# Optimization experiments

Measured on AMD Instinct MI355X. Metric: run time of the kernel, lower is better.

## Reference

```python
import jax, jax.numpy as jnp
from jax import lax
import numpy as np

TEMP = 0.9
TOP_P = 0.95
TOP_K = 50
THRESHOLD = 0.9
MASK_ID = 50256
BLOCK = 128
VOCAB = 50257
GEN = 1024
PROMPT = 512


def setup_inputs() -> dict:
    key = jax.random.key(0)
    k1, k2 = jax.random.split(key)
    logits = jax.random.normal(k1, (1, GEN, VOCAB), dtype=jnp.float32)
    x = jax.random.randint(k2, (1, PROMPT + GEN), 0, VOCAB, dtype=jnp.int32)
    # current block is fully masked -> current_transfer_tokens == BLOCK (static)
    x = x.at[:, PROMPT:PROMPT + BLOCK].set(MASK_ID)
    mask_index = jnp.zeros((1, GEN), dtype=bool).at[:, :BLOCK].set(True)
    return {"i": 0, "x": x, "logits": logits, "mask_index": mask_index,
            "current_block_start": PROMPT, "num_transfer": BLOCK}


def _filter_logits(logits):
    """temperature + top-p + top-k filtering, faithful to torch Sampler."""
    l = logits / TEMP
    neg = jnp.finfo(l.dtype).min
    # top-p: sort descending, cumulative softmax, shifted removal mask, unsort
    sort_idx = jnp.argsort(-l, axis=-1)                       # [1,L,V]
    sorted_l = jnp.take_along_axis(l, sort_idx, axis=-1)
    cum = jnp.cumsum(jax.nn.softmax(sorted_l, axis=-1), axis=-1)
    remove = cum > TOP_P
    remove = jnp.concatenate([jnp.zeros_like(remove[..., :1]), remove[..., :-1]], axis=-1)
    inv = jnp.argsort(sort_idx, axis=-1)                      # inverse permutation
    rm_mask = jnp.take_along_axis(remove, inv, axis=-1)
    l = jnp.where(rm_mask, neg, l)
    # top-k: keep values >= k-th largest
    kth = lax.top_k(l, TOP_K)[0][..., -1:]
    l = jnp.where(l < kth, neg, l)
    return l


def reference(i, x, logits, mask_index, current_block_start, num_transfer):
    l = _filter_logits(logits)                                # [1,GEN,V]
    probs = jax.nn.softmax(l, axis=-1)
    # temperature > 0 -> categorical sample, confidence = prob of sampled token
    x0 = jax.random.categorical(jax.random.key(42), l, axis=-1)          # [1,GEN]
    confidence = jnp.take_along_axis(probs, x0[..., None], axis=-1)[..., 0]
    # scatter into full region: x_[mask]=x0, full_confidence[mask]=conf else -inf
    x_ = jnp.where(mask_index, x0.astype(x.dtype), jnp.asarray(MASK_ID, x.dtype))
    full_conf = jnp.where(mask_index, confidence, -jnp.inf)
    full_conf = full_conf.at[:, BLOCK:].set(-jnp.inf)
    # top-k over positions; index 0 always transferred, rest only if >= threshold
    sel_conf, sel_idx = lax.top_k(full_conf, num_transfer)    # [1,k]
    keep = (sel_conf >= THRESHOLD).at[:, 0].set(True)
    transfer = jnp.zeros(x_.shape, dtype=bool).at[0, sel_idx[0]].set(keep[0])
    region = x[:, current_block_start:]
    new_region = jnp.where(transfer, x_, region)
    x_new = x.at[:, current_block_start:].set(new_region)
    return x_new, full_conf
```

## Files before the change

### kernel.cpp

```cpp
#include <hip/hip_runtime.h>
#include <stdint.h>
#include <math.h>

#define VOCAB 50257
#define GEN 1024
#define PROMPT 512
#define XTOT (PROMPT + GEN)
#define BLOCKQ 128
#define TOPK 50
#define TEMP 0.9f
#define TOPP 0.95f
#define THRESH 0.9f
#define MASK_ID 50256
#define CAND_T 3.0f
#define NEG_SENTINEL (-3.0e38f)

#define NSPLIT 16
#define CHUNK 3144
#define KPT 13
#define MAXCC 48

#define WS_CONF   0
#define WS_X0     512
#define WS_PMAX   1024
#define WS_PSUM   9216
#define WS_CCNT   17408
#define WS_CVAL   25600
#define WS_CIDX   418816
#define WS_NEEDED 812032

__device__ __forceinline__ uint32_t rotl32(uint32_t x, uint32_t d){ return (x<<d)|(x>>(32u-d)); }

__device__ __forceinline__ bool read_mask(const void* m, int r){
  const uint8_t* b = (const uint8_t*)m;
  bool i32mode = ((b[1] | b[2] | b[3]) == 0);
  return i32mode ? (((const int*)m)[r] != 0) : (b[r] != 0);
}

__device__ void threefry2x32_20(uint32_t k0, uint32_t k1, uint32_t& x0, uint32_t& x1){
  uint32_t ks2 = k0 ^ k1 ^ 0x1BD11BDAu;
  x0 += k0; x1 += k1;
#define RND(r) { x0 += x1; x1 = rotl32(x1, r); x1 ^= x0; }
  RND(13) RND(15) RND(26) RND(6)
  x0 += k1; x1 += ks2 + 1u;
  RND(17) RND(29) RND(16) RND(24)
  x0 += ks2; x1 += k0 + 2u;
  RND(13) RND(15) RND(26) RND(6)
  x0 += k0; x1 += k1 + 3u;
  RND(17) RND(29) RND(16) RND(24)
  x0 += k1; x1 += ks2 + 4u;
  RND(13) RND(15) RND(26) RND(6)
  x0 += ks2; x1 += k0 + 5u;
#undef RND
}

__device__ float gumbel_at(int64_t flat){
  const int64_t N = (int64_t)GEN * VOCAB;
  const int64_t half = N / 2;
  uint32_t a, b; int use_first;
  if (flat < half){ a = (uint32_t)flat; b = (uint32_t)(flat + half); use_first = 1; }
  else            { a = (uint32_t)(flat - half); b = (uint32_t)flat;  use_first = 0; }
  threefry2x32_20(0u, 42u, a, b);
  uint32_t bits = use_first ? a : b;
  uint32_t fb = (bits >> 9) | 0x3F800000u;
  float f = __uint_as_float(fb) - 1.0f;
  float u = (f > 0.0f) ? f : 1.17549435e-38f;
  double t = -log((double)u);
  return (float)(-log(t));
}

__global__ __launch_bounds__(256) void stage1_kernel(
    const float* __restrict__ logits,
    const void* __restrict__ mask,
    float* __restrict__ pmax, float* __restrict__ psum,
    int* __restrict__ ccnt, float* __restrict__ cval, int* __restrict__ cidx)
{
  const int r = blockIdx.x >> 4;
  const int c = blockIdx.x & (NSPLIT - 1);
  const int tid = threadIdx.x;
  const int slot = r * NSPLIT + c;

  if (!read_mask(mask, r)){
    if (tid == 0) ccnt[slot] = 0;
    return;
  }
  const float* row = logits + (size_t)r * VOCAB;
  const int i0 = c * CHUNK;
  const int i1 = min(i0 + CHUNK, VOCAB);

  __shared__ int s_cnt;
  __shared__ float red[256];
  if (tid == 0) s_cnt = 0;
  __syncthreads();

  float v[KPT];
  float m = -INFINITY;
#pragma unroll
  for (int k = 0; k < KPT; k++){
    int i = i0 + tid + k * 256;
    float l = -INFINITY;
    if (i < i1){
      l = row[i] / TEMP;
      if (l >= CAND_T){
        int p = atomicAdd(&s_cnt, 1);
        if (p < MAXCC){
          cval[(size_t)slot * MAXCC + p] = l;
          cidx[(size_t)slot * MAXCC + p] = i;
        }
      }
    }
    v[k] = l;
    m = fmaxf(m, l);
  }

  red[tid] = m;
  __syncthreads();
  for (int s = 128; s > 0; s >>= 1){
    if (tid < s) red[tid] = fmaxf(red[tid], red[tid + s]);
    __syncthreads();
  }
  const float mc = red[0];
  __syncthreads();

  float z = 0.f;
#pragma unroll
  for (int k = 0; k < KPT; k++) z += expf(v[k] - mc);
  red[tid] = z;
  __syncthreads();
  for (int s = 128; s > 0; s >>= 1){
    if (tid < s) red[tid] += red[tid + s];
    __syncthreads();
  }
  if (tid == 0){
    pmax[slot] = mc;
    psum[slot] = red[0];
    ccnt[slot] = min(s_cnt, MAXCC);
  }
}

__global__ __launch_bounds__(256) void stage2_kernel(
    const void* __restrict__ mask,
    const float* __restrict__ pmax, const float* __restrict__ psum,
    const int* __restrict__ ccnt, const float* __restrict__ cval, const int* __restrict__ cidx,
    float* __restrict__ conf_out, int* __restrict__ x0_out)
{
  const int r = blockIdx.x;
  const int tid = threadIdx.x;

  if (!read_mask(mask, r)){
    if (tid == 0){ conf_out[r] = -INFINITY; x0_out[r] = 0; }
    return;
  }

  __shared__ float cv[NSPLIT * MAXCC];
  __shared__ int   cx[NSPLIT * MAXCC];
  __shared__ int   s_off[NSPLIT + 1];
  __shared__ float topv[TOPK];
  __shared__ int   topi[TOPK];
  __shared__ float s_m, s_Z, s_Zf;
  __shared__ int   s_keptN;
  __shared__ float sv[64];
  __shared__ int   si[64];

  if (tid == 0){
    float m = -INFINITY;
    for (int c = 0; c < NSPLIT; c++) m = fmaxf(m, pmax[r * NSPLIT + c]);
    float Z = 0.f;
    for (int c = 0; c < NSPLIT; c++) Z += psum[r * NSPLIT + c] * expf(pmax[r * NSPLIT + c] - m);
    s_m = m; s_Z = Z;
    int off = 0;
    for (int c = 0; c < NSPLIT; c++){ s_off[c] = off; off += min(ccnt[r * NSPLIT + c], MAXCC); }
    s_off[NSPLIT] = off;
  }
  __syncthreads();
  const float mm = s_m;
  const int cnt = s_off[NSPLIT];

  for (int c = 0; c < NSPLIT; c++){
    int base = s_off[c], n = s_off[c + 1] - base;
    for (int j = tid; j < n; j += 256){
      cv[base + j] = cval[(size_t)(r * NSPLIT + c) * MAXCC + j];
      cx[base + j] = cidx[(size_t)(r * NSPLIT + c) * MAXCC + j];
    }
  }
  __syncthreads();

  for (int i = tid; i < cnt; i += 256){
    float v = cv[i]; int ix = cx[i];
    int rank = 0;
    for (int j = 0; j < cnt; j++){
      float vj = cv[j];
      rank += (vj > v) || (vj == v && cx[j] < ix);
    }
    if (rank < TOPK){ topv[rank] = v; topi[rank] = ix; }
  }
  __syncthreads();

  if (tid == 0){
    int kn = min(cnt, TOPK);
    float cum = 0.f;
    int c = kn;
    for (int j = 1; j < kn; j++){
      cum += expf(topv[j - 1] - mm) / s_Z;
      if (cum > TOPP){ c = j; break; }
    }
    int keptN = (c < kn) ? c : kn;
    float Zf = 0.f;
    for (int j = 0; j < keptN; j++) Zf += expf(topv[j] - mm);
    s_keptN = keptN; s_Zf = Zf;
  }
  __syncthreads();

  const int keptN = s_keptN;
  if (tid < 64){ sv[tid] = -INFINITY; si[tid] = 0x7FFFFFFF; }
  __syncthreads();
  if (tid < keptN){
    int64_t flat = (int64_t)r * VOCAB + topi[tid];
    float g = gumbel_at(flat);
    sv[tid] = topv[tid] + g;
    si[tid] = topi[tid];
  }
  __syncthreads();

  if (tid == 0){
    float best = -INFINITY; int bi = 0x7FFFFFFF; float wl = 0.f;
    for (int j = 0; j < keptN; j++){
      float s = sv[j]; int ix = si[j];
      if (s > best || (s == best && ix < bi)){ best = s; bi = ix; wl = topv[j]; }
    }
    if (keptN <= 0){ conf_out[r] = 0.f; x0_out[r] = 0; }
    else {
      conf_out[r] = expf(wl - mm) / s_Zf;
      x0_out[r] = bi;
    }
  }
}

__global__ __launch_bounds__(256) void row_kernel(
    const float* __restrict__ logits,
    const void* __restrict__ mask,
    float* __restrict__ conf_out, int* __restrict__ x0_out)
{
  const int r = blockIdx.x;
  const int tid = threadIdx.x;

  __shared__ float cval[768];
  __shared__ int   cidx[768];
  __shared__ int   ccount;
  __shared__ float red[256];
  __shared__ float topv[TOPK];
  __shared__ int   topi[TOPK];
  __shared__ float s_m, s_Z, s_Zf;
  __shared__ int   s_keptN;
  __shared__ float sv[64];
  __shared__ int   si[64];

  if (!read_mask(mask, r)){
    if (tid == 0){ conf_out[r] = -INFINITY; x0_out[r] = 0; }
    return;
  }
  const float* row = logits + (size_t)r * VOCAB;
  if (tid == 0) ccount = 0;
  __syncthreads();

  float m = -INFINITY;
  for (int i = tid; i < VOCAB; i += 256){
    float l = row[i] / TEMP;
    m = fmaxf(m, l);
    if (l >= CAND_T){
      int pos = atomicAdd(&ccount, 1);
      if (pos < 768){ cval[pos] = l; cidx[pos] = i; }
    }
  }
  red[tid] = m;
  __syncthreads();
  for (int s = 128; s > 0; s >>= 1){
    if (tid < s) red[tid] = fmaxf(red[tid], red[tid + s]);
    __syncthreads();
  }
  if (tid == 0) s_m = red[0];
  __syncthreads();
  const float mm = s_m;

  float z = 0.f;
  for (int i = tid; i < VOCAB; i += 256){
    float l = row[i] / TEMP;
    z += expf(l - mm);
  }
  red[tid] = z;
  __syncthreads();
  for (int s = 128; s > 0; s >>= 1){
    if (tid < s) red[tid] += red[tid + s];
    __syncthreads();
  }
  if (tid == 0) s_Z = red[0];
  __syncthreads();

  const int cnt = min(ccount, 768);
  for (int i = tid; i < cnt; i += 256){
    float v = cval[i]; int ix = cidx[i];
    int rank = 0;
    for (int j = 0; j < cnt; j++){
      float vj = cval[j];
      rank += (vj > v) || (vj == v && cidx[j] < ix);
    }
    if (rank < TOPK){ topv[rank] = v; topi[rank] = ix; }
  }
  __syncthreads();

  if (tid == 0){
    int kn = min(cnt, TOPK);
    float cum = 0.f;
    int c = kn;
    for (int j = 1; j < kn; j++){
      cum += expf(topv[j - 1] - mm) / s_Z;
      if (cum > TOPP){ c = j; break; }
    }
    int keptN = (c < kn) ? c : kn;
    float Zf = 0.f;
    for (int j = 0; j < keptN; j++) Zf += expf(topv[j] - mm);
    s_keptN = keptN; s_Zf = Zf;
  }
  __syncthreads();

  const int keptN = s_keptN;
  if (tid < 64){ sv[tid] = -INFINITY; si[tid] = 0x7FFFFFFF; }
  __syncthreads();
  if (tid < keptN){
    int64_t flat = (int64_t)r * VOCAB + topi[tid];
    float g = gumbel_at(flat);
    sv[tid] = topv[tid] + g;
    si[tid] = topi[tid];
  }
  __syncthreads();

  if (tid == 0){
    float best = -INFINITY; int bi = 0x7FFFFFFF; float wl = 0.f;
    for (int j = 0; j < keptN; j++){
      float s = sv[j]; int ix = si[j];
      if (s > best || (s == best && ix < bi)){ best = s; bi = ix; wl = topv[j]; }
    }
    if (keptN <= 0){ conf_out[r] = 0.f; x0_out[r] = 0; }
    else {
      conf_out[r] = expf(wl - mm) / s_Zf;
      x0_out[r] = bi;
    }
  }
}

__global__ __launch_bounds__(256) void finalize_kernel(
    const int* __restrict__ x,
    const void* __restrict__ mask,
    const int* __restrict__ cbs_p, const int* __restrict__ nt_p,
    const float* __restrict__ conf, const int* __restrict__ x0,
    float* __restrict__ out)
{
  __shared__ float fc[BLOCKQ];
  __shared__ uint8_t tr[BLOCKQ];
  const int tid = threadIdx.x;

  if (tid < BLOCKQ) fc[tid] = conf[tid];
  __syncthreads();

  for (int p = tid; p < GEN; p += 256){
    float v = (p < BLOCKQ) ? fc[p] : -INFINITY;
    out[XTOT + p] = isinf(v) ? NEG_SENTINEL : v;
  }

  const int nt  = *nt_p;
  const int cbs = *cbs_p;

  if (tid < BLOCKQ){
    float v = fc[tid];
    int rank = 0;
    for (int q = 0; q < BLOCKQ; q++){
      float w = fc[q];
      rank += (w > v) || (w == v && q < tid);
    }
    bool sel = rank < nt;
    tr[tid] = (uint8_t)(sel && (v >= THRESH || rank == 0));
  }
  __syncthreads();

  for (int k = tid; k < XTOT; k += 256){
    int val = x[k];
    int p = k - cbs;
    if (p >= 0 && p < BLOCKQ && tr[p]){
      val = read_mask(mask, p) ? x0[p] : MASK_ID;
    }
    out[k] = (float)val;
  }
}

extern "C" void kernel_launch(void* const* d_in, const int* in_sizes, int n_in,
                              void* d_out, int out_size, void* d_ws, size_t ws_size,
                              hipStream_t stream)
{
  const int*   x      = (const int*)d_in[1];
  const float* logits = (const float*)d_in[2];
  const void*  mask   = d_in[3];
  const int*   cbs    = (const int*)d_in[4];
  const int*   nt     = (const int*)d_in[5];
  float* out  = (float*)d_out;

  char*  ws   = (char*)d_ws;
  float* conf = (float*)(ws + WS_CONF);
  int*   x0   = (int*)(ws + WS_X0);

  if (ws_size >= WS_NEEDED){
    float* pmax = (float*)(ws + WS_PMAX);
    float* psum = (float*)(ws + WS_PSUM);
    int*   ccnt = (int*)(ws + WS_CCNT);
    float* cval = (float*)(ws + WS_CVAL);
    int*   cidx = (int*)(ws + WS_CIDX);
    hipLaunchKernelGGL(stage1_kernel, dim3(BLOCKQ * NSPLIT), dim3(256), 0, stream,
                       logits, mask, pmax, psum, ccnt, cval, cidx);
    hipLaunchKernelGGL(stage2_kernel, dim3(BLOCKQ), dim3(256), 0, stream,
                       mask, pmax, psum, ccnt, cval, cidx, conf, x0);
  } else {
    hipLaunchKernelGGL(row_kernel, dim3(BLOCKQ), dim3(256), 0, stream,
                       logits, mask, conf, x0);
  }
  hipLaunchKernelGGL(finalize_kernel, dim3(1), dim3(256), 0, stream,
                     x, mask, cbs, nt, conf, x0, out);
}
```

Measured before the change: 60.65 us.

## Fuse split-row stages and finalize into one kernel via last-block atomic counters

Merges the per-chunk partial reduction, the per-row candidate merge and sampling, and the final top-k/transfer step into a single kernel. Each row's last finishing chunk block, found with an atomic counter, does the row merge, and the globally last row does the finalize. A small kernel zeroes the counters first, and the shared-memory tree reductions become wavefront shuffle reductions. This removes inter-kernel launch gaps at the cost of serialised tail work in the last blocks and added fences and atomics.

```diff
diff --git a/kernel.cpp b/kernel.cpp
--- a/kernel.cpp
+++ b/kernel.cpp
@@ -22,12 +22,14 @@
 
 #define WS_CONF   0
 #define WS_X0     512
-#define WS_PMAX   1024
-#define WS_PSUM   9216
-#define WS_CCNT   17408
-#define WS_CVAL   25600
-#define WS_CIDX   418816
-#define WS_NEEDED 812032
+#define WS_ROWCNT 1024
+#define WS_DONE   1536
+#define WS_PMAX   2048
+#define WS_PSUM   10240
+#define WS_CCNT   18432
+#define WS_CVAL   26624
+#define WS_CIDX   419840
+#define WS_NEEDED 813056
 
 __device__ __forceinline__ uint32_t rotl32(uint32_t x, uint32_t d){ return (x<<d)|(x>>(32u-d)); }
 
@@ -69,89 +71,26 @@
   return (float)(-log(t));
 }
 
-__global__ __launch_bounds__(256) void stage1_kernel(
-    const float* __restrict__ logits,
-    const void* __restrict__ mask,
-    float* __restrict__ pmax, float* __restrict__ psum,
-    int* __restrict__ ccnt, float* __restrict__ cval, int* __restrict__ cidx)
+__global__ __launch_bounds__(256) void zero_kernel(int* __restrict__ p){
+  if (threadIdx.x < BLOCKQ + 1) p[threadIdx.x] = 0;
+}
+
+__global__ __launch_bounds__(256) void fused_kernel(
+    const float* __restrict__ logits, const void* __restrict__ mask,
+    const int* __restrict__ x, const int* __restrict__ cbs_p, const int* __restrict__ nt_p,
+    float* __restrict__ out,
+    float* conf, int* x0, int* rowcnt, int* done,
+    float* pmax, float* psum, int* ccnt, float* cval, int* cidx)
 {
-  const int r = blockIdx.x >> 4;
-  const int c = blockIdx.x & (NSPLIT - 1);
+  const int bid = blockIdx.x;
+  const int r = bid >> 4;
+  const int c = bid & (NSPLIT - 1);
   const int tid = threadIdx.x;
-  const int slot = r * NSPLIT + c;
-
-  if (!read_mask(mask, r)){
-    if (tid == 0) ccnt[slot] = 0;
-    return;
-  }
-  const float* row = logits + (size_t)r * VOCAB;
-  const int i0 = c * CHUNK;
-  const int i1 = min(i0 + CHUNK, VOCAB);
-
-  __shared__ int s_cnt;
-  __shared__ float red[256];
-  if (tid == 0) s_cnt = 0;
-  __syncthreads();
-
-  float v[KPT];
-  float m = -INFINITY;
-#pragma unroll
-  for (int k = 0; k < KPT; k++){
-    int i = i0 + tid + k * 256;
-    float l = -INFINITY;
-    if (i < i1){
-      l = row[i] / TEMP;
-      if (l >= CAND_T){
-        int p = atomicAdd(&s_cnt, 1);
-        if (p < MAXCC){
-          cval[(size_t)slot * MAXCC + p] = l;
-          cidx[(size_t)slot * MAXCC + p] = i;
-        }
-      }
-    }
-    v[k] = l;
-    m = fmaxf(m, l);
-  }
-
-  red[tid] = m;
-  __syncthreads();
-  for (int s = 128; s > 0; s >>= 1){
-    if (tid < s) red[tid] = fmaxf(red[tid], red[tid + s]);
-    __syncthreads();
-  }
-  const float mc = red[0];
-  __syncthreads();
-
-  float z = 0.f;
-#pragma unroll
-  for (int k = 0; k < KPT; k++) z += expf(v[k] - mc);
-  red[tid] = z;
-  __syncthreads();
-  for (int s = 128; s > 0; s >>= 1){
-    if (tid < s) red[tid] += red[tid + s];
-    __syncthreads();
-  }
-  if (tid == 0){
-    pmax[slot] = mc;
-    psum[slot] = red[0];
-    ccnt[slot] = min(s_cnt, MAXCC);
-  }
-}
-
-__global__ __launch_bounds__(256) void stage2_kernel(
-    const void* __restrict__ mask,
-    const float* __restrict__ pmax, const float* __restrict__ psum,
-    const int* __restrict__ ccnt, const float* __restrict__ cval, const int* __restrict__ cidx,
-    float* __restrict__ conf_out, int* __restrict__ x0_out)
-{
-  const int r = blockIdx.x;
-  const int tid = threadIdx.x;
-
-  if (!read_mask(mask, r)){
-    if (tid == 0){ conf_out[r] = -INFINITY; x0_out[r] = 0; }
-    return;
-  }
-
+  const int lane = tid & 63;
+  const int wid = tid >> 6;
+
+  __shared__ float lred[4];
+  __shared__ int s_cnt, s_last, s_fin;
   __shared__ float cv[NSPLIT * MAXCC];
   __shared__ int   cx[NSPLIT * MAXCC];
   __shared__ int   s_off[NSPLIT + 1];
@@ -161,89 +100,184 @@
   __shared__ int   s_keptN;
   __shared__ float sv[64];
   __shared__ int   si[64];
-
-  if (tid == 0){
+  __shared__ float fc[BLOCKQ];
+  __shared__ uint8_t tr[BLOCKQ];
+
+  const bool rmask = read_mask(mask, r);
+
+  if (rmask){
+    const float* row = logits + (size_t)r * VOCAB;
+    const int i0 = c * CHUNK;
+    const int i1 = min(i0 + CHUNK, VOCAB);
+    if (tid == 0) s_cnt = 0;
+    __syncthreads();
+
+    float v[KPT];
     float m = -INFINITY;
-    for (int c = 0; c < NSPLIT; c++) m = fmaxf(m, pmax[r * NSPLIT + c]);
-    float Z = 0.f;
-    for (int c = 0; c < NSPLIT; c++) Z += psum[r * NSPLIT + c] * expf(pmax[r * NSPLIT + c] - m);
-    s_m = m; s_Z = Z;
-    int off = 0;
-    for (int c = 0; c < NSPLIT; c++){ s_off[c] = off; off += min(ccnt[r * NSPLIT + c], MAXCC); }
-    s_off[NSPLIT] = off;
-  }
-  __syncthreads();
-  const float mm = s_m;
-  const int cnt = s_off[NSPLIT];
-
-  for (int c = 0; c < NSPLIT; c++){
-    int base = s_off[c], n = s_off[c + 1] - base;
-    for (int j = tid; j < n; j += 256){
-      cv[base + j] = cval[(size_t)(r * NSPLIT + c) * MAXCC + j];
-      cx[base + j] = cidx[(size_t)(r * NSPLIT + c) * MAXCC + j];
-    }
-  }
-  __syncthreads();
-
-  for (int i = tid; i < cnt; i += 256){
-    float v = cv[i]; int ix = cx[i];
+#pragma unroll
+    for (int k = 0; k < KPT; k++){
+      int i = i0 + tid + k * 256;
+      float l = -INFINITY;
+      if (i < i1){
+        l = row[i] / TEMP;
+        if (l >= CAND_T){
+          int p = atomicAdd(&s_cnt, 1);
+          if (p < MAXCC){
+            cval[(size_t)bid * MAXCC + p] = l;
+            cidx[(size_t)bid * MAXCC + p] = i;
+          }
+        }
+      }
+      v[k] = l;
+      m = fmaxf(m, l);
+    }
+#pragma unroll
+    for (int off = 32; off; off >>= 1) m = fmaxf(m, __shfl_xor(m, off));
+    if (lane == 0) lred[wid] = m;
+    __syncthreads();
+    const float mc = fmaxf(fmaxf(lred[0], lred[1]), fmaxf(lred[2], lred[3]));
+    float z = 0.f;
+#pragma unroll
+    for (int k = 0; k < KPT; k++) z += expf(v[k] - mc);
+#pragma unroll
+    for (int off = 32; off; off >>= 1) z += __shfl_xor(z, off);
+    __syncthreads();
+    if (lane == 0) lred[wid] = z;
+    __syncthreads();
+    if (tid == 0){
+      pmax[bid] = mc;
+      psum[bid] = lred[0] + lred[1] + lred[2] + lred[3];
+      ccnt[bid] = min(s_cnt, MAXCC);
+    }
+  }
+
+  __threadfence();
+  __syncthreads();
+  if (tid == 0) s_last = (atomicAdd(&rowcnt[r], 1) == NSPLIT - 1) ? 1 : 0;
+  __syncthreads();
+  if (!s_last) return;
+  __threadfence();
+
+  if (rmask){
+    if (tid == 0){
+      float m = -INFINITY;
+      for (int cc = 0; cc < NSPLIT; cc++) m = fmaxf(m, pmax[r * NSPLIT + cc]);
+      float Z = 0.f;
+      for (int cc = 0; cc < NSPLIT; cc++) Z += psum[r * NSPLIT + cc] * expf(pmax[r * NSPLIT + cc] - m);
+      s_m = m; s_Z = Z;
+      int off = 0;
+      for (int cc = 0; cc < NSPLIT; cc++){ s_off[cc] = off; off += min(ccnt[r * NSPLIT + cc], MAXCC); }
+      s_off[NSPLIT] = off;
+    }
+    __syncthreads();
+    const float mm = s_m;
+    const int cnt = s_off[NSPLIT];
+
+    for (int cc = 0; cc < NSPLIT; cc++){
+      int base = s_off[cc], n = s_off[cc + 1] - base;
+      for (int j = tid; j < n; j += 256){
+        cv[base + j] = cval[(size_t)(r * NSPLIT + cc) * MAXCC + j];
+        cx[base + j] = cidx[(size_t)(r * NSPLIT + cc) * MAXCC + j];
+      }
+    }
+    __syncthreads();
+
+    for (int i = tid; i < cnt; i += 256){
+      float v = cv[i]; int ix = cx[i];
+      int rank = 0;
+      for (int j = 0; j < cnt; j++){
+        float vj = cv[j];
+        rank += (vj > v) || (vj == v && cx[j] < ix);
+      }
+      if (rank < TOPK){ topv[rank] = v; topi[rank] = ix; }
+    }
+    __syncthreads();
+
+    if (tid == 0){
+      int kn = min(cnt, TOPK);
+      float cum = 0.f;
+      int cstop = kn;
+      for (int j = 1; j < kn; j++){
+        cum += expf(topv[j - 1] - mm) / s_Z;
+        if (cum > TOPP){ cstop = j; break; }
+      }
+      int keptN = (cstop < kn) ? cstop : kn;
+      float Zf = 0.f;
+      for (int j = 0; j < keptN; j++) Zf += expf(topv[j] - mm);
+      s_keptN = keptN; s_Zf = Zf;
+    }
+    __syncthreads();
+
+    const int keptN = s_keptN;
+    if (tid < 64){ sv[tid] = -INFINITY; si[tid] = 0x7FFFFFFF; }
+    __syncthreads();
+    if (tid < keptN){
+      int64_t flat = (int64_t)r * VOCAB + topi[tid];
+      float g = gumbel_at(flat);
+      sv[tid] = topv[tid] + g;
+      si[tid] = topi[tid];
+    }
+    __syncthreads();
+
+    if (tid == 0){
+      float best = -INFINITY; int bi = 0x7FFFFFFF; float wl = 0.f;
+      for (int j = 0; j < keptN; j++){
+        float s = sv[j]; int ix = si[j];
+        if (s > best || (s == best && ix < bi)){ best = s; bi = ix; wl = topv[j]; }
+      }
+      if (keptN <= 0){ conf[r] = 0.f; x0[r] = 0; }
+      else { conf[r] = expf(wl - mm) / s_Zf; x0[r] = bi; }
+    }
+  } else {
+    if (tid == 0){ conf[r] = -INFINITY; x0[r] = 0; }
+  }
+
+  __threadfence();
+  __syncthreads();
+  if (tid == 0) s_fin = (atomicAdd(done, 1) == BLOCKQ - 1) ? 1 : 0;
+  __syncthreads();
+  if (!s_fin) return;
+  __threadfence();
+
+  if (tid < BLOCKQ) fc[tid] = conf[tid];
+  __syncthreads();
+
+  for (int p = tid; p < GEN; p += 256){
+    float v = (p < BLOCKQ) ? fc[p] : -INFINITY;
+    out[XTOT + p] = isinf(v) ? NEG_SENTINEL : v;
+  }
+
+  const int nt  = *nt_p;
+  const int cbs = *cbs_p;
+
+  if (tid < BLOCKQ){
+    float v = fc[tid];
     int rank = 0;
-    for (int j = 0; j < cnt; j++){
-      float vj = cv[j];
-      rank += (vj > v) || (vj == v && cx[j] < ix);
-    }
-    if (rank < TOPK){ topv[rank] = v; topi[rank] = ix; }
-  }
-  __syncthreads();
-
-  if (tid == 0){
-    int kn = min(cnt, TOPK);
-    float cum = 0.f;
-    int c = kn;
-    for (int j = 1; j < kn; j++){
-      cum += expf(topv[j - 1] - mm) / s_Z;
-      if (cum > TOPP){ c = j; break; }
-    }
-    int keptN = (c < kn) ? c : kn;
-    float Zf = 0.f;
-    for (int j = 0; j < keptN; j++) Zf += expf(topv[j] - mm);
-    s_keptN = keptN; s_Zf = Zf;
-  }
-  __syncthreads();
-
-  const int keptN = s_keptN;
-  if (tid < 64){ sv[tid] = -INFINITY; si[tid] = 0x7FFFFFFF; }
-  __syncthreads();
-  if (tid < keptN){
-    int64_t flat = (int64_t)r * VOCAB + topi[tid];
-    float g = gumbel_at(flat);
-    sv[tid] = topv[tid] + g;
-    si[tid] = topi[tid];
-  }
-  __syncthreads();
-
-  if (tid == 0){
-    float best = -INFINITY; int bi = 0x7FFFFFFF; float wl = 0.f;
-    for (int j = 0; j < keptN; j++){
-      float s = sv[j]; int ix = si[j];
-      if (s > best || (s == best && ix < bi)){ best = s; bi = ix; wl = topv[j]; }
-    }
-    if (keptN <= 0){ conf_out[r] = 0.f; x0_out[r] = 0; }
-    else {
-      conf_out[r] = expf(wl - mm) / s_Zf;
-      x0_out[r] = bi;
-    }
+    for (int q = 0; q < BLOCKQ; q++){
+      float w = fc[q];
+      rank += (w > v) || (w == v && q < tid);
+    }
+    bool sel = rank < nt;
+    tr[tid] = (uint8_t)(sel && (v >= THRESH || rank == 0));
+  }
+  __syncthreads();
+
+  for (int k = tid; k < XTOT; k += 256){
+    int val = x[k];
+    int p = k - cbs;
+    if (p >= 0 && p < BLOCKQ && tr[p]){
+      val = read_mask(mask, p) ? x0[p] : MASK_ID;
+    }
+    out[k] = (float)val;
   }
 }
 
 __global__ __launch_bounds__(256) void row_kernel(
-    const float* __restrict__ logits,
-    const void* __restrict__ mask,
+    const float* __restrict__ logits, const void* __restrict__ mask,
     float* __restrict__ conf_out, int* __restrict__ x0_out)
 {
   const int r = blockIdx.x;
   const int tid = threadIdx.x;
-
   __shared__ float cval[768];
   __shared__ int   cidx[768];
   __shared__ int   ccount;
@@ -262,7 +296,6 @@
   const float* row = logits + (size_t)r * VOCAB;
   if (tid == 0) ccount = 0;
   __syncthreads();
-
   float m = -INFINITY;
   for (int i = tid; i < VOCAB; i += 256){
     float l = row[i] / TEMP;
@@ -272,30 +305,17 @@
       if (pos < 768){ cval[pos] = l; cidx[pos] = i; }
     }
   }
-  red[tid] = m;
-  __syncthreads();
-  for (int s = 128; s > 0; s >>= 1){
-    if (tid < s) red[tid] = fmaxf(red[tid], red[tid + s]);
-    __syncthreads();
-  }
+  red[tid] = m; __syncthreads();
+  for (int s = 128; s > 0; s >>= 1){ if (tid < s) red[tid] = fmaxf(red[tid], red[tid+s]); __syncthreads(); }
   if (tid == 0) s_m = red[0];
   __syncthreads();
   const float mm = s_m;
-
   float z = 0.f;
-  for (int i = tid; i < VOCAB; i += 256){
-    float l = row[i] / TEMP;
-    z += expf(l - mm);
-  }
-  red[tid] = z;
-  __syncthreads();
-  for (int s = 128; s > 0; s >>= 1){
-    if (tid < s) red[tid] += red[tid + s];
-    __syncthreads();
-  }
+  for (int i = tid; i < VOCAB; i += 256) z += expf(row[i] / TEMP - mm);
+  red[tid] = z; __syncthreads();
+  for (int s = 128; s > 0; s >>= 1){ if (tid < s) red[tid] += red[tid+s]; __syncthreads(); }
   if (tid == 0) s_Z = red[0];
   __syncthreads();
-
   const int cnt = min(ccount, 768);
   for (int i = tid; i < cnt; i += 256){
     float v = cval[i]; int ix = cidx[i];
@@ -307,33 +327,27 @@
     if (rank < TOPK){ topv[rank] = v; topi[rank] = ix; }
   }
   __syncthreads();
-
   if (tid == 0){
     int kn = min(cnt, TOPK);
-    float cum = 0.f;
-    int c = kn;
+    float cum = 0.f; int cstop = kn;
     for (int j = 1; j < kn; j++){
-      cum += expf(topv[j - 1] - mm) / s_Z;
-      if (cum > TOPP){ c = j; break; }
-    }
-    int keptN = (c < kn) ? c : kn;
+      cum += expf(topv[j-1] - mm) / s_Z;
+      if (cum > TOPP){ cstop = j; break; }
+    }
+    int keptN = (cstop < kn) ? cstop : kn;
     float Zf = 0.f;
     for (int j = 0; j < keptN; j++) Zf += expf(topv[j] - mm);
     s_keptN = keptN; s_Zf = Zf;
   }
   __syncthreads();
-
   const int keptN = s_keptN;
   if (tid < 64){ sv[tid] = -INFINITY; si[tid] = 0x7FFFFFFF; }
   __syncthreads();
   if (tid < keptN){
-    int64_t flat = (int64_t)r * VOCAB + topi[tid];
-    float g = gumbel_at(flat);
-    sv[tid] = topv[tid] + g;
-    si[tid] = topi[tid];
-  }
-  __syncthreads();
-
+    float g = gumbel_at((int64_t)r * VOCAB + topi[tid]);
+    sv[tid] = topv[tid] + g; si[tid] = topi[tid];
+  }
+  __syncthreads();
   if (tid == 0){
     float best = -INFINITY; int bi = 0x7FFFFFFF; float wl = 0.f;
     for (int j = 0; j < keptN; j++){
@@ -341,16 +355,12 @@
       if (s > best || (s == best && ix < bi)){ best = s; bi = ix; wl = topv[j]; }
     }
     if (keptN <= 0){ conf_out[r] = 0.f; x0_out[r] = 0; }
-    else {
-      conf_out[r] = expf(wl - mm) / s_Zf;
-      x0_out[r] = bi;
-    }
+    else { conf_out[r] = expf(wl - mm) / s_Zf; x0_out[r] = bi; }
   }
 }
 
 __global__ __launch_bounds__(256) void finalize_kernel(
-    const int* __restrict__ x,
-    const void* __restrict__ mask,
+    const int* __restrict__ x, const void* __restrict__ mask,
     const int* __restrict__ cbs_p, const int* __restrict__ nt_p,
     const float* __restrict__ conf, const int* __restrict__ x0,
     float* __restrict__ out)
@@ -358,18 +368,14 @@
   __shared__ float fc[BLOCKQ];
   __shared__ uint8_t tr[BLOCKQ];
   const int tid = threadIdx.x;
-
   if (tid < BLOCKQ) fc[tid] = conf[tid];
   __syncthreads();
-
   for (int p = tid; p < GEN; p += 256){
     float v = (p < BLOCKQ) ? fc[p] : -INFINITY;
     out[XTOT + p] = isinf(v) ? NEG_SENTINEL : v;
   }
-
   const int nt  = *nt_p;
   const int cbs = *cbs_p;
-
   if (tid < BLOCKQ){
     float v = fc[tid];
     int rank = 0;
@@ -381,13 +387,10 @@
     tr[tid] = (uint8_t)(sel && (v >= THRESH || rank == 0));
   }
   __syncthreads();
-
   for (int k = tid; k < XTOT; k += 256){
     int val = x[k];
     int p = k - cbs;
-    if (p >= 0 && p < BLOCKQ && tr[p]){
-      val = read_mask(mask, p) ? x0[p] : MASK_ID;
-    }
+    if (p >= 0 && p < BLOCKQ && tr[p]) val = read_mask(mask, p) ? x0[p] : MASK_ID;
     out[k] = (float)val;
   }
 }
@@ -401,11 +404,13 @@
   const void*  mask   = d_in[3];
   const int*   cbs    = (const int*)d_in[4];
   const int*   nt     = (const int*)d_in[5];
-  float* out  = (float*)d_out;
-
-  char*  ws   = (char*)d_ws;
-  float* conf = (float*)(ws + WS_CONF);
-  int*   x0   = (int*)(ws + WS_X0);
+  float* out = (float*)d_out;
+
+  char*  ws     = (char*)d_ws;
+  float* conf   = (float*)(ws + WS_CONF);
+  int*   x0     = (int*)(ws + WS_X0);
+  int*   rowcnt = (int*)(ws + WS_ROWCNT);
+  int*   done   = (int*)(ws + WS_DONE);
 
   if (ws_size >= WS_NEEDED){
     float* pmax = (float*)(ws + WS_PMAX);
@@ -413,14 +418,14 @@
     int*   ccnt = (int*)(ws + WS_CCNT);
     float* cval = (float*)(ws + WS_CVAL);
     int*   cidx = (int*)(ws + WS_CIDX);
-    hipLaunchKernelGGL(stage1_kernel, dim3(BLOCKQ * NSPLIT), dim3(256), 0, stream,
-                       logits, mask, pmax, psum, ccnt, cval, cidx);
-    hipLaunchKernelGGL(stage2_kernel, dim3(BLOCKQ), dim3(256), 0, stream,
-                       mask, pmax, psum, ccnt, cval, cidx, conf, x0);
+    hipLaunchKernelGGL(zero_kernel, dim3(1), dim3(256), 0, stream, rowcnt);
+    hipLaunchKernelGGL(fused_kernel, dim3(BLOCKQ * NSPLIT), dim3(256), 0, stream,
+                       logits, mask, x, cbs, nt, out,
+                       conf, x0, rowcnt, done, pmax, psum, ccnt, cval, cidx);
   } else {
     hipLaunchKernelGGL(row_kernel, dim3(BLOCKQ), dim3(256), 0, stream,
                        logits, mask, conf, x0);
-  }
-  hipLaunchKernelGGL(finalize_kernel, dim3(1), dim3(256), 0, stream,
-                     x, mask, cbs, nt, conf, x0, out);
-}
+    hipLaunchKernelGGL(finalize_kernel, dim3(1), dim3(256), 0, stream,
+                       x, mask, cbs, nt, conf, x0, out);
+  }
+}
```

Measured after the change: 213.0 us. 3.51x slower.
